# Performance work log

Hardware: AMD Instinct MI355X
Metric: run time of the kernel (lower is better)

## Reference

```python
import jax, jax.numpy as jnp
import numpy as np

N_NODES = 50000
N_EDGES = 800000
N_GRAPHS = 64
EMB_DIM = 24
N_KERNELS = 2
M_DIM = 64
FOURIER = 4
POS_DIM = 3
EDGE_IN = 2 * FOURIER + 1 + 2 * EMB_DIM  # 57
MLP_DIM = 256
N_OUT = 4
FFNN_IN = EMB_DIM * (N_KERNELS + 1)  # 72


def _lin(key, fan_in, fan_out, stack=None):
    # xavier-uniform weight, zero bias (matches weights_init)
    lim = (6.0 / (fan_in + fan_out)) ** 0.5
    shp = ((stack,) if stack else ()) + (fan_in, fan_out)
    w = jax.random.uniform(key, shp, minval=-lim, maxval=lim, dtype=jnp.float32)
    b = jnp.zeros(((stack,) if stack else ()) + (fan_out,), jnp.float32)
    return w, b


def setup_inputs() -> dict:
    key = jax.random.key(0)
    ks = jax.random.split(key, 20)
    z = jax.random.randint(ks[0], (N_NODES,), 0, 22)
    pos = jax.random.normal(ks[1], (N_NODES, POS_DIM), jnp.float32)
    edge_index = jax.random.randint(ks[2], (2, N_EDGES), 0, N_NODES)
    batch_idx = jnp.sort(jax.random.randint(ks[3], (N_NODES,), 0, N_GRAPHS))
    lim_e = (6.0 / (22 + EMB_DIM)) ** 0.5
    emb_table = jax.random.uniform(ks[4], (22, EMB_DIM), minval=-lim_e, maxval=lim_e, dtype=jnp.float32)
    emb_w, emb_b = _lin(ks[5], EMB_DIM, EMB_DIM)
    # EGNN kernel params, stacked over N_KERNELS
    ew1, eb1 = _lin(ks[6], EDGE_IN, EDGE_IN * 2, N_KERNELS)
    ew2, eb2 = _lin(ks[7], EDGE_IN * 2, M_DIM, N_KERNELS)
    cw1, cb1 = _lin(ks[8], M_DIM, M_DIM * 4, N_KERNELS)
    cw2, cb2 = _lin(ks[9], M_DIM * 4, 1, N_KERNELS)
    nw1, nb1 = _lin(ks[10], EMB_DIM + M_DIM, EMB_DIM * 2, N_KERNELS)
    nw2, nb2 = _lin(ks[11], EMB_DIM * 2, EMB_DIM, N_KERNELS)
    # ffnn: Linear(72,256), Linear(256,256), Linear(256,256), Linear(256,4)
    f0w, f0b = _lin(ks[12], FFNN_IN, MLP_DIM)
    f1w, f1b = _lin(ks[13], MLP_DIM, MLP_DIM)
    f2w, f2b = _lin(ks[14], MLP_DIM, MLP_DIM)
    fow, fob = _lin(ks[15], MLP_DIM, N_OUT)
    return dict(z=z, pos=pos, edge_index=edge_index, batch_idx=batch_idx,
                emb_table=emb_table, emb_w=emb_w, emb_b=emb_b,
                ew1=ew1, eb1=eb1, ew2=ew2, eb2=eb2,
                cw1=cw1, cb1=cb1, cw2=cw2, cb2=cb2,
                nw1=nw1, nb1=nb1, nw2=nw2, nb2=nb2,
                f0w=f0w, f0b=f0b, f1w=f1w, f1b=f1b, f2w=f2w, f2b=f2b,
                fow=fow, fob=fob)


def _egnn_layer(feats, coors, src, dst, ew1, eb1, ew2, eb2, cw1, cb1, cw2, cb2, nw1, nb1, nw2, nb2):
    # EGNN_sparse (PyG flow source_to_target: i=dst=edge_index[1], j=src=edge_index[0])
    rel = coors[src] - coors[dst]                       # [E,3]
    d = jnp.sum(rel * rel, axis=-1, keepdims=True)      # [E,1] squared distance
    scales = 2.0 ** jnp.arange(FOURIER, dtype=feats.dtype)
    ds = d / scales                                     # [E,4]
    edge_feat = jnp.concatenate([jnp.sin(ds), jnp.cos(ds), d], axis=-1)  # [E,9]
    e_in = jnp.concatenate([feats[dst], feats[src], edge_feat], axis=-1)  # [E,57]
    m_ij = jax.nn.silu(jax.nn.silu(e_in @ ew1 + eb1) @ ew2 + eb2)         # [E,64]
    coor_w = jax.nn.silu(m_ij @ cw1 + cb1) @ cw2 + cb2                    # [E,1]
    coors_out = coors + jax.ops.segment_sum(coor_w * rel, dst, num_segments=N_NODES)
    m_i = jax.ops.segment_sum(m_ij, dst, num_segments=N_NODES)            # [N,64]
    h = jax.nn.silu(jnp.concatenate([feats, m_i], axis=-1) @ nw1 + nb1)
    feats_out = feats + (h @ nw2 + nb2)
    return feats_out, coors_out


def reference(z, pos, edge_index, batch_idx, emb_table, emb_w, emb_b,
              ew1, eb1, ew2, eb2, cw1, cb1, cw2, cb2, nw1, nb1, nw2, nb2,
              f0w, f0b, f1w, f1b, f2w, f2b, fow, fob):
    src, dst = edge_index[0], edge_index[1]
    feats = emb_table[z] @ emb_w + emb_b
    coors = pos
    flist = [feats]
    for k in range(N_KERNELS):
        feats, coors = _egnn_layer(feats, coors, src, dst,
                                   ew1[k], eb1[k], ew2[k], eb2[k],
                                   cw1[k], cb1[k], cw2[k], cb2[k],
                                   nw1[k], nb1[k], nw2[k], nb2[k])
        flist.append(feats)
    x = jax.nn.silu(jnp.concatenate(flist, axis=-1))     # [N,72]
    x = jax.nn.silu(x @ f0w + f0b)
    x = jax.nn.silu(x @ f1w + f1b)
    x = jax.nn.silu(x @ f2w + f2b)                       # [N,256]
    cnt = jax.ops.segment_sum(jnp.ones((x.shape[0],), x.dtype), batch_idx, num_segments=N_GRAPHS)
    pooled = jax.ops.segment_sum(x, batch_idx, num_segments=N_GRAPHS) / jnp.maximum(cnt, 1.0)[:, None]
    return jax.nn.sigmoid(pooled @ fow + fob)            # [B,4]
```

## Files before the change

kernel.cpp:

```cpp
#include <hip/hip_runtime.h>
#include <hip/hip_bf16.h>

#define N_NODES  50000
#define N_EDGES  800000
#define N_GRAPHS 64
#define EMB      24
#define MDIM     64
#define EDGE_IN  57
#define EH       114
#define CH       256
#define NIN      88
#define NH       48
#define MLP      256
#define ETILE    128
#define NTILE    64

typedef __bf16 bf16_t;
typedef __bf16 bf16x8 __attribute__((ext_vector_type(8)));
typedef __bf16 bf16x4 __attribute__((ext_vector_type(4)));
typedef float  f32x4  __attribute__((ext_vector_type(4)));

__device__ __forceinline__ float siluf(float x) {
    return x * __builtin_amdgcn_rcpf(1.0f + __expf(-x));
}

__global__ void embed_kernel(const int* __restrict__ z, const float* __restrict__ table,
                             const float* __restrict__ w, const float* __restrict__ b,
                             const int* __restrict__ batch, float* __restrict__ f0,
                             bf16_t* __restrict__ fb0, float* __restrict__ cnt)
{
    int n = blockIdx.x * blockDim.x + threadIdx.x;
    if (n >= N_NODES) return;
    float r[EMB];
    const float4* tr = reinterpret_cast<const float4*>(table + z[n] * EMB);
    #pragma unroll
    for (int q = 0; q < 6; q++) {
        float4 v = tr[q];
        r[q*4] = v.x; r[q*4+1] = v.y; r[q*4+2] = v.z; r[q*4+3] = v.w;
    }
    float o[EMB];
    #pragma unroll
    for (int j = 0; j < EMB; j++) o[j] = b[j];
    #pragma unroll
    for (int i = 0; i < EMB; i++) {
        #pragma unroll
        for (int j = 0; j < EMB; j++) o[j] = fmaf(r[i], w[i*EMB + j], o[j]);
    }
    float4* dst = reinterpret_cast<float4*>(f0 + (size_t)n * EMB);
    #pragma unroll
    for (int q = 0; q < 6; q++) dst[q] = make_float4(o[q*4], o[q*4+1], o[q*4+2], o[q*4+3]);
    bf16x8* bdst = reinterpret_cast<bf16x8*>(fb0 + (size_t)n * EMB);
    #pragma unroll
    for (int q = 0; q < 3; q++) {
        bf16x8 pk;
        #pragma unroll
        for (int j = 0; j < 8; j++) pk[j] = (bf16_t)o[q*8 + j];
        bdst[q] = pk;
    }
    atomicAdd(&cnt[batch[n]], 1.0f);
}

#define PK_W1   (128*64)
#define PK_W2   (64*128)
#define PK_CW   (256*64)
#define PK_F0   (256*128)
#define PK_FM   (256*256)
#define PK_TOT  (2*PK_W1 + 2*PK_W2 + PK_CW + PK_F0 + 2*PK_FM)
__global__ void pack_kernel(const float* __restrict__ ew1, const float* __restrict__ eb1,
                            const float* __restrict__ ew2, const float* __restrict__ eb2,
                            const float* __restrict__ cw1, const float* __restrict__ f0w,
                            const float* __restrict__ f1w, const float* __restrict__ f2w,
                            bf16_t* __restrict__ pw)
{
    int idx = blockIdx.x * blockDim.x + threadIdx.x;
    if (idx >= PK_TOT) return;
    float v = 0.0f;
    if (idx < 2 * PK_W1) {
        int l = idx / PK_W1, r = idx - l * PK_W1;
        int n = r >> 6, k = r & 63;
        if (n < EH && k < EDGE_IN)       v = ew1[(l * EDGE_IN + k) * EH + n];
        else if (n < EH && k == EDGE_IN) v = eb1[l * EH + n];
    } else if (idx < 2 * PK_W1 + 2 * PK_W2) {
        int r0 = idx - 2 * PK_W1;
        int l = r0 / PK_W2, r = r0 - l * PK_W2;
        int n = r >> 7, k = r & 127;
        if (k < EH)       v = ew2[(l * EH + k) * MDIM + n];
        else if (k == EH) v = eb2[l * MDIM + n];
    } else if (idx < 2 * PK_W1 + 2 * PK_W2 + PK_CW) {
        int r = idx - (2 * PK_W1 + 2 * PK_W2);
        int n = r >> 6, k = r & 63;
        v = cw1[k * CH + n];
    } else if (idx < 2 * PK_W1 + 2 * PK_W2 + PK_CW + PK_F0) {
        int r = idx - (2 * PK_W1 + 2 * PK_W2 + PK_CW);
        int n = r >> 7, k = r & 127;
        if (k < 72) v = f0w[k * MLP + n];
    } else {
        int r0 = idx - (2 * PK_W1 + 2 * PK_W2 + PK_CW + PK_F0);
        int l = r0 / PK_FM, r = r0 - l * PK_FM;
        int n = r >> 8, k = r & 255;
        v = (l == 0) ? f1w[k * MLP + n] : f2w[k * MLP + n];
    }
    pw[idx] = (bf16_t)v;
}

__global__ void hist_kernel(const int* __restrict__ dst, int* __restrict__ deg)
{
    int e = blockIdx.x * blockDim.x + threadIdx.x;
    if (e < N_EDGES) atomicAdd(&deg[dst[e]], 1);
}

__global__ __launch_bounds__(1024)
void scan_kernel(const int* __restrict__ deg, int* __restrict__ cursor)
{
    __shared__ int part[1024];
    int t = threadIdx.x;
    const int PER = 49;
    int base = t * PER;
    int s = 0;
    for (int i = 0; i < PER; i++) {
        int p = base + i;
        if (p < N_NODES) s += deg[p];
    }
    part[t] = s;
    __syncthreads();
    for (int off = 1; off < 1024; off <<= 1) {
        int add = (t >= off) ? part[t - off] : 0;
        __syncthreads();
        part[t] += add;
        __syncthreads();
    }
    int run = (t > 0) ? part[t - 1] : 0;
    for (int i = 0; i < PER; i++) {
        int p = base + i;
        if (p < N_NODES) { cursor[p] = run; run += deg[p]; }
    }
}

__global__ void scatter_kernel(const int* __restrict__ src, const int* __restrict__ dst,
                               int* __restrict__ cursor, int* __restrict__ srcs_s,
                               int* __restrict__ dsts_s)
{
    int e = blockIdx.x * blockDim.x + threadIdx.x;
    if (e >= N_EDGES) return;
    int d = dst[e];
    int pos = atomicAdd(&cursor[d], 1);
    srcs_s[pos] = src[e];
    dsts_s[pos] = d;
}

template<int COOR>
__global__ __launch_bounds__(256, 4)
void edge_mfma(const bf16_t* __restrict__ fb, const float* __restrict__ coors,
               const int* __restrict__ srcs_s, const int* __restrict__ dsts_s,
               const bf16_t* __restrict__ W1t, const bf16_t* __restrict__ W2t,
               const bf16_t* __restrict__ CW1t, const float* __restrict__ cb1,
               const float* __restrict__ cw2, const float* __restrict__ cb2,
               float* __restrict__ m_i, float* __restrict__ cdelta)
{
    __shared__ __align__(16) char R1raw[ETILE * 64 * 4];
    __shared__ float s_rel[COOR ? ETILE * 3 : 4];
    __shared__ float s_cacc[COOR ? ETILE : 4];
    __shared__ int   s_dst[ETILE];
    bf16_t* R1 = (bf16_t*)R1raw;
    float*  Mf32 = (float*)R1raw;

    const int t = threadIdx.x;
    const int w = t >> 6;
    const int l = t & 63;
    const int row0 = w * 32;
    const int ebase = blockIdx.x * ETILE;
    const int l15 = l & 15, l4 = l >> 4;

    {
        int e_loc = t >> 1, half = t & 1;
        int e = ebase + e_loc;
        int s = srcs_s[e], d = dsts_s[e];
        if (half == 0) {
            s_dst[e_loc] = d;
            const bf16x8* fp = reinterpret_cast<const bf16x8*>(fb + (size_t)d * EMB);
            #pragma unroll
            for (int g = 0; g < 3; g++)
                *(bf16x8*)&R1[e_loc*64 + (g ^ (e_loc & 7))*8] = fp[g];
        } else {
            const bf16x8* fp = reinterpret_cast<const bf16x8*>(fb + (size_t)s * EMB);
            #pragma unroll
            for (int g = 0; g < 3; g++)
                *(bf16x8*)&R1[e_loc*64 + ((g + 3) ^ (e_loc & 7))*8] = fp[g];
            float rx = coors[s*3+0] - coors[d*3+0];
            float ry = coors[s*3+1] - coors[d*3+1];
            float rz = coors[s*3+2] - coors[d*3+2];
            float d2 = rx*rx + ry*ry + rz*rz;
            if (COOR) { s_rel[e_loc*3+0] = rx; s_rel[e_loc*3+1] = ry; s_rel[e_loc*3+2] = rz; }
            bf16x8 p6, p7;
            p6[0]=(bf16_t)__sinf(d2);        p6[1]=(bf16_t)__sinf(d2*0.5f);
            p6[2]=(bf16_t)__sinf(d2*0.25f);  p6[3]=(bf16_t)__sinf(d2*0.125f);
            p6[4]=(bf16_t)__cosf(d2);        p6[5]=(bf16_t)__cosf(d2*0.5f);
            p6[6]=(bf16_t)__cosf(d2*0.25f);  p6[7]=(bf16_t)__cosf(d2*0.125f);
            p7[0]=(bf16_t)d2; p7[1]=(bf16_t)1.0f;
            p7[2]=(bf16_t)0.f; p7[3]=(bf16_t)0.f; p7[4]=(bf16_t)0.f;
            p7[5]=(bf16_t)0.f; p7[6]=(bf16_t)0.f; p7[7]=(bf16_t)0.f;
            *(bf16x8*)&R1[e_loc*64 + (6 ^ (e_loc & 7))*8] = p6;
            *(bf16x8*)&R1[e_loc*64 + (7 ^ (e_loc & 7))*8] = p7;
        }
    }
    __syncthreads();

    f32x4 acc1[2][8];
    #pragma unroll
    for (int et = 0; et < 2; et++)
        #pragma unroll
        for (int ft = 0; ft < 8; ft++) acc1[et][ft] = (f32x4){0.f,0.f,0.f,0.f};
    #pragma unroll
    for (int ks = 0; ks < 2; ks++) {
        bf16x8 bfrag[2];
        #pragma unroll
        for (int et = 0; et < 2; et++) {
            int e = row0 + et*16 + l15;
            bfrag[et] = *(const bf16x8*)&R1[e*64 + ((ks*4 + l4) ^ (e & 7))*8];
        }
        #pragma unroll
        for (int ft = 0; ft < 8; ft++) {
            bf16x8 a = *(const bf16x8*)&W1t[(ft*16 + l15)*64 + (ks*4 + l4)*8];
            acc1[0][ft] = __builtin_amdgcn_mfma_f32_16x16x32_bf16(a, bfrag[0], acc1[0][ft], 0, 0, 0);
            acc1[1][ft] = __builtin_amdgcn_mfma_f32_16x16x32_bf16(a, bfrag[1], acc1[1][ft], 0, 0, 0);
        }
    }
    __syncthreads();
    #pragma unroll
    for (int et = 0; et < 2; et++)
        #pragma unroll
        for (int ft = 0; ft < 8; ft++) {
            int e = row0 + et*16 + l15;
            int f0 = ft*16 + l4*4;
            bf16x4 pk;
            #pragma unroll
            for (int r4 = 0; r4 < 4; r4++) {
                float hv = siluf(acc1[et][ft][r4]);
                if (f0 + r4 == EH) hv = 1.0f;
                pk[r4] = (bf16_t)hv;
            }
            *(bf16x4*)&R1[e*128 + ((f0 >> 3) ^ (e & 7))*8 + (f0 & 7)] = pk;
        }
    __syncthreads();

    f32x4 acc2[2][4];
    #pragma unroll
    for (int et = 0; et < 2; et++)
        #pragma unroll
        for (int ft = 0; ft < 4; ft++) acc2[et][ft] = (f32x4){0.f,0.f,0.f,0.f};
    #pragma unroll
    for (int ks = 0; ks < 4; ks++) {
        bf16x8 bfrag[2];
        #pragma unroll
        for (int et = 0; et < 2; et++) {
            int e = row0 + et*16 + l15;
            bfrag[et] = *(const bf16x8*)&R1[e*128 + ((ks*4 + l4) ^ (e & 7))*8];
        }
        #pragma unroll
        for (int ft = 0; ft < 4; ft++) {
            bf16x8 a = *(const bf16x8*)&W2t[(ft*16 + l15)*128 + (ks*4 + l4)*8];
            acc2[0][ft] = __builtin_amdgcn_mfma_f32_16x16x32_bf16(a, bfrag[0], acc2[0][ft], 0, 0, 0);
            acc2[1][ft] = __builtin_amdgcn_mfma_f32_16x16x32_bf16(a, bfrag[1], acc2[1][ft], 0, 0, 0);
        }
    }
    __syncthreads();
    #pragma unroll
    for (int et = 0; et < 2; et++)
        #pragma unroll
        for (int ft = 0; ft < 4; ft++) {
            int e = row0 + et*16 + l15;
            int f0 = ft*16 + l4*4;
            f32x4 v;
            #pragma unroll
            for (int r4 = 0; r4 < 4; r4++) v[r4] = siluf(acc2[et][ft][r4]);
            *(f32x4*)&Mf32[e*64 + (((f0 >> 2) ^ (e & 7)) << 2)] = v;
        }
    __syncthreads();

    {
        int col = t & 63;
        int gsw_base = col >> 2, cw = col & 3;
        int gb = w * 32;
        int cur = s_dst[gb];
        float run = 0.f;
        for (int i = 0; i < 32; i++) {
            int row = gb + i;
            int d = s_dst[row];
            float v = Mf32[row*64 + ((gsw_base ^ (row & 7)) << 2) + cw];
            if (d != cur) { atomicAdd(&m_i[(size_t)cur*64 + col], run); run = 0.f; cur = d; }
            run += v;
        }
        atomicAdd(&m_i[(size_t)cur*64 + col], run);
    }

    if (COOR) {
        float csum[2] = {0.f, 0.f};
        #pragma unroll
        for (int half = 0; half < 2; half++) {
            f32x4 acc3[2][8];
            #pragma unroll
            for (int et = 0; et < 2; et++)
                #pragma unroll
                for (int ft = 0; ft < 8; ft++) acc3[et][ft] = (f32x4){0.f,0.f,0.f,0.f};
            #pragma unroll
            for (int ks = 0; ks < 2; ks++) {
                bf16x8 bfrag[2];
                #pragma unroll
                for (int et = 0; et < 2; et++) {
                    int e = row0 + et*16 + l15;
                    int g0 = (ks*4 + l4) * 2;
                    f32x4 lo = *(const f32x4*)&Mf32[e*64 + ((g0 ^ (e & 7)) << 2)];
                    f32x4 hi = *(const f32x4*)&Mf32[e*64 + (((g0 + 1) ^ (e & 7)) << 2)];
                    bf16x8 bk;
                    #pragma unroll
                    for (int j = 0; j < 4; j++) { bk[j] = (bf16_t)lo[j]; bk[j+4] = (bf16_t)hi[j]; }
                    bfrag[et] = bk;
                }
                #pragma unroll
                for (int ft = 0; ft < 8; ft++) {
                    bf16x8 a = *(const bf16x8*)&CW1t[(half*128 + ft*16 + l15)*64 + (ks*4 + l4)*8];
                    acc3[0][ft] = __builtin_amdgcn_mfma_f32_16x16x32_bf16(a, bfrag[0], acc3[0][ft], 0, 0, 0);
                    acc3[1][ft] = __builtin_amdgcn_mfma_f32_16x16x32_bf16(a, bfrag[1], acc3[1][ft], 0, 0, 0);
                }
            }
            #pragma unroll
            for (int ft = 0; ft < 8; ft++) {
                int f0 = half*128 + ft*16 + l4*4;
                float4 c1 = *(const float4*)&cb1[f0];
                float4 w2 = *(const float4*)&cw2[f0];
                #pragma unroll
                for (int et = 0; et < 2; et++) {
                    csum[et] = fmaf(siluf(acc3[et][ft][0] + c1.x), w2.x, csum[et]);
                    csum[et] = fmaf(siluf(acc3[et][ft][1] + c1.y), w2.y, csum[et]);
                    csum[et] = fmaf(siluf(acc3[et][ft][2] + c1.z), w2.z, csum[et]);
                    csum[et] = fmaf(siluf(acc3[et][ft][3] + c1.w), w2.w, csum[et]);
                }
            }
        }
        #pragma unroll
        for (int et = 0; et < 2; et++) {
            csum[et] += __shfl_xor(csum[et], 16);
            csum[et] += __shfl_xor(csum[et], 32);
        }
        if (l < 16) {
            float cb2v = cb2[0];
            s_cacc[row0 + l]      = csum[0] + cb2v;
            s_cacc[row0 + 16 + l] = csum[1] + cb2v;
        }
        __syncthreads();
        if (t < ETILE) {
            int d = s_dst[t];
            bool head = (t == 0) || (s_dst[t-1] != d);
            if (head) {
                float ax = 0.f, ay = 0.f, az = 0.f;
                int i = t;
                do {
                    float c = s_cacc[i];
                    ax = fmaf(c, s_rel[i*3+0], ax);
                    ay = fmaf(c, s_rel[i*3+1], ay);
                    az = fmaf(c, s_rel[i*3+2], az);
                    ++i;
                } while (i < ETILE && s_dst[i] == d);
                atomicAdd(&cdelta[d*3+0], ax);
                atomicAdd(&cdelta[d*3+1], ay);
                atomicAdd(&cdelta[d*3+2], az);
            }
        }
    }
}

template<int EMIT_BF16>
__global__ __launch_bounds__(256)
void node_kernel(const float* __restrict__ feats, const float* __restrict__ m_i,
                 const float* __restrict__ nw1, const float* __restrict__ nb1,
                 const float* __restrict__ nw2, const float* __restrict__ nb2,
                 float* __restrict__ fout, bf16_t* __restrict__ fbout)
{
    __shared__ float s_w1t[NH * NIN];
    __shared__ float s_b1[NH];
    __shared__ float s_w2[NH * EMB];
    __shared__ float s_b2[EMB];
    const int tid = threadIdx.x;
    for (int idx = tid; idx < NH * NIN; idx += 256) {
        int k = idx / NIN, i = idx - k * NIN;
        s_w1t[idx] = nw1[i * NH + k];
    }
    for (int idx = tid; idx < NH * EMB; idx += 256) s_w2[idx] = nw2[idx];
    if (tid < NH) s_b1[tid] = nb1[tid];
    if (tid < EMB) s_b2[tid] = nb2[tid];
    __syncthreads();

    int n = blockIdx.x * 256 + tid;
    if (n >= N_NODES) return;

    float in[NIN];
    const float4* fp = reinterpret_cast<const float4*>(feats + (size_t)n * EMB);
    #pragma unroll
    for (int q = 0; q < 6; q++) {
        float4 v = fp[q];
        in[q*4] = v.x; in[q*4+1] = v.y; in[q*4+2] = v.z; in[q*4+3] = v.w;
    }
    const float4* mp = reinterpret_cast<const float4*>(m_i + (size_t)n * MDIM);
    #pragma unroll
    for (int q = 0; q < 16; q++) {
        float4 v = mp[q];
        in[EMB+q*4] = v.x; in[EMB+q*4+1] = v.y; in[EMB+q*4+2] = v.z; in[EMB+q*4+3] = v.w;
    }
    float o[EMB];
    #pragma unroll
    for (int j = 0; j < EMB; j++) o[j] = in[j] + s_b2[j];
    for (int k = 0; k < NH; k++) {
        const float* w1 = &s_w1t[k * NIN];
        float a0 = 0.f, a1 = 0.f, a2 = 0.f, a3 = 0.f;
        #pragma unroll
        for (int i = 0; i < NIN; i += 4) {
            a0 = fmaf(in[i],   w1[i],   a0);
            a1 = fmaf(in[i+1], w1[i+1], a1);
            a2 = fmaf(in[i+2], w1[i+2], a2);
            a3 = fmaf(in[i+3], w1[i+3], a3);
        }
        float h = siluf(s_b1[k] + ((a0 + a1) + (a2 + a3)));
        const float* w2 = &s_w2[k * EMB];
        #pragma unroll
        for (int j = 0; j < EMB; j++) o[j] = fmaf(h, w2[j], o[j]);
    }
    float4* dst = reinterpret_cast<float4*>(fout + (size_t)n * EMB);
    #pragma unroll
    for (int q = 0; q < 6; q++) dst[q] = make_float4(o[q*4], o[q*4+1], o[q*4+2], o[q*4+3]);
    if (EMIT_BF16) {
        bf16x8* bdst = reinterpret_cast<bf16x8*>(fbout + (size_t)n * EMB);
        #pragma unroll
        for (int q = 0; q < 3; q++) {
            bf16x8 pk;
            #pragma unroll
            for (int j = 0; j < 8; j++) pk[j] = (bf16_t)o[q*8 + j];
            bdst[q] = pk;
        }
    }
}

__global__ void coor_kernel(const float* __restrict__ pos, const float* __restrict__ cdelta,
                            float* __restrict__ out)
{
    int i = blockIdx.x * blockDim.x + threadIdx.x;
    if (i < N_NODES * 3) out[i] = pos[i] + cdelta[i];
}

__global__ __launch_bounds__(512, 4)
void ffnn_fused(const float* __restrict__ f0, const float* __restrict__ f1,
                const float* __restrict__ f2,
                const bf16_t* __restrict__ W0p, const bf16_t* __restrict__ W1p,
                const bf16_t* __restrict__ W2p,
                const float* __restrict__ b0, const float* __restrict__ b1,
                const float* __restrict__ b2,
                const int* __restrict__ batch, float* __restrict__ pooled)
{
    __shared__ __align__(16) bf16_t sH[NTILE * 256];
    __shared__ int s_batch[NTILE];
    const int t = threadIdx.x;
    const int w = t >> 6, l = t & 63;
    const int l15 = l & 15, q = l >> 4;
    const int mt = w & 3;
    const int nh = w >> 2;
    const int mrow0 = mt * 16;
    const int n0 = blockIdx.x * NTILE;

    {
        int row = t >> 3, part = t & 7;
        int n = n0 + row;
        bool valid = n < N_NODES;
        if (part == 7) s_batch[row] = valid ? batch[n] : -1;
        #pragma unroll
        for (int gi = 0; gi < 2; gi++) {
            int g = part * 2 + gi;
            bf16x8 pk;
            #pragma unroll
            for (int j = 0; j < 8; j++) pk[j] = (bf16_t)0.f;
            if (valid && g < 9) {
                const float* sp = (g < 3) ? f0 + (size_t)n*EMB + 8*g
                                : (g < 6) ? f1 + (size_t)n*EMB + 8*(g-3)
                                          : f2 + (size_t)n*EMB + 8*(g-6);
                float4 a = ((const float4*)sp)[0], b = ((const float4*)sp)[1];
                pk[0]=(bf16_t)siluf(a.x); pk[1]=(bf16_t)siluf(a.y);
                pk[2]=(bf16_t)siluf(a.z); pk[3]=(bf16_t)siluf(a.w);
                pk[4]=(bf16_t)siluf(b.x); pk[5]=(bf16_t)siluf(b.y);
                pk[6]=(bf16_t)siluf(b.z); pk[7]=(bf16_t)siluf(b.w);
            }
            *(bf16x8*)&sH[row*128 + (g ^ (row & 7))*8] = pk;
        }
    }
    __syncthreads();

    bf16x8 a0[4];
    {
        int r = mrow0 + l15;
        #pragma unroll
        for (int ks = 0; ks < 4; ks++)
            a0[ks] = *(const bf16x8*)&sH[r*128 + ((ks*4 + q) ^ (r & 7))*8];
    }
    __syncthreads();

    f32x4 acc[8];
    #pragma unroll
    for (int nt = 0; nt < 8; nt++) {
        float bv = b0[(nh*8 + nt)*16 + l15];
        acc[nt] = (f32x4){bv, bv, bv, bv};
    }
    #pragma unroll
    for (int ks = 0; ks < 4; ks++)
        #pragma unroll
        for (int nt = 0; nt < 8; nt++) {
            int n = (nh*8 + nt)*16 + l15;
            bf16x8 b = *(const bf16x8*)&W0p[n*128 + (ks*4 + q)*8];
            acc[nt] = __builtin_amdgcn_mfma_f32_16x16x32_bf16(a0[ks], b, acc[nt], 0, 0, 0);
        }
    #pragma unroll
    for (int nt = 0; nt < 8; nt++)
        #pragma unroll
        for (int r4 = 0; r4 < 4; r4++) {
            int row = mrow0 + q*4 + r4;
            int col = (nh*8 + nt)*16 + l15;
            sH[row*256 + ((col >> 3) ^ (row & 7))*8 + (col & 7)] = (bf16_t)siluf(acc[nt][r4]);
        }
    __syncthreads();

    #pragma unroll
    for (int layer = 0; layer < 2; layer++) {
        const bf16_t* Wp = layer ? W2p : W1p;
        const float*  bb = layer ? b2  : b1;
        #pragma unroll
        for (int nt = 0; nt < 8; nt++) {
            float bv = bb[(nh*8 + nt)*16 + l15];
            acc[nt] = (f32x4){bv, bv, bv, bv};
        }
        for (int ks = 0; ks < 8; ks++) {
            int r = mrow0 + l15;
            bf16x8 a = *(const bf16x8*)&sH[r*256 + ((ks*4 + q) ^ (r & 7))*8];
            #pragma unroll
            for (int nt = 0; nt < 8; nt++) {
                int n = (nh*8 + nt)*16 + l15;
                bf16x8 b = *(const bf16x8*)&Wp[n*256 + (ks*4 + q)*8];
                acc[nt] = __builtin_amdgcn_mfma_f32_16x16x32_bf16(a, b, acc[nt], 0, 0, 0);
            }
        }
        __syncthreads();
        #pragma unroll
        for (int nt = 0; nt < 8; nt++)
            #pragma unroll
            for (int r4 = 0; r4 < 4; r4++) {
                int row = mrow0 + q*4 + r4;
                int col = (nh*8 + nt)*16 + l15;
                sH[row*256 + ((col >> 3) ^ (row & 7))*8 + (col & 7)] = (bf16_t)siluf(acc[nt][r4]);
            }
        __syncthreads();
    }

    {
        int j = t & 255;
        int rh = t >> 8;
        int g = j >> 3, jo = j & 7;
        int cur = -1;
        float run = 0.f;
        for (int i = rh*32; i < rh*32 + 32; i++) {
            int bb = s_batch[i];
            if (bb != cur) {
                if (cur >= 0) atomicAdd(&pooled[cur * MLP + j], run);
                run = 0.f; cur = bb;
            }
            if (bb >= 0) run += (float)sH[i*256 + (g ^ (i & 7))*8 + jo];
        }
        if (cur >= 0) atomicAdd(&pooled[cur * MLP + j], run);
    }
}

__global__ void final_kernel(const float* __restrict__ pooled, const float* __restrict__ cnt,
                             const float* __restrict__ fow, const float* __restrict__ fob,
                             float* __restrict__ out)
{
    int t = threadIdx.x;
    int bg = t >> 2, o = t & 3;
    float c = fmaxf(cnt[bg], 1.0f);
    float acc = 0.f;
    for (int i = 0; i < MLP; i++) acc = fmaf(pooled[bg * MLP + i], fow[i * 4 + o], acc);
    acc = acc / c + fob[o];
    out[t] = 1.0f / (1.0f + __expf(-acc));
}

extern "C" void kernel_launch(void* const* d_in, const int* in_sizes, int n_in,
                              void* d_out, int out_size, void* d_ws, size_t ws_size,
                              hipStream_t stream)
{
    const int*   z     = (const int*)  d_in[0];
    const float* pos   = (const float*)d_in[1];
    const int*   eidx  = (const int*)  d_in[2];
    const int*   batch = (const int*)  d_in[3];
    const float* embt  = (const float*)d_in[4];
    const float* embw  = (const float*)d_in[5];
    const float* embb  = (const float*)d_in[6];
    const float* ew1   = (const float*)d_in[7];
    const float* eb1   = (const float*)d_in[8];
    const float* ew2   = (const float*)d_in[9];
    const float* eb2   = (const float*)d_in[10];
    const float* cw1   = (const float*)d_in[11];
    const float* cb1   = (const float*)d_in[12];
    const float* cw2   = (const float*)d_in[13];
    const float* cb2   = (const float*)d_in[14];
    const float* nw1   = (const float*)d_in[15];
    const float* nb1   = (const float*)d_in[16];
    const float* nw2   = (const float*)d_in[17];
    const float* nb2   = (const float*)d_in[18];
    const float* f0w   = (const float*)d_in[19];
    const float* f0b   = (const float*)d_in[20];
    const float* f1w   = (const float*)d_in[21];
    const float* f1b   = (const float*)d_in[22];
    const float* f2w   = (const float*)d_in[23];
    const float* f2b   = (const float*)d_in[24];
    const float* fow   = (const float*)d_in[25];
    const float* fob   = (const float*)d_in[26];

    float* ws     = (float*)d_ws;
    float* f0     = ws;
    float* f1v    = f0 + (size_t)N_NODES * EMB;
    float* f2v    = f1v + (size_t)N_NODES * EMB;
    bf16_t* fb0   = (bf16_t*)(f2v + (size_t)N_NODES * EMB);
    bf16_t* fb1   = fb0 + (size_t)N_NODES * EMB;
    float* coorsA = (float*)(fb1 + (size_t)N_NODES * EMB);
    float* cdelta = coorsA + N_NODES * 3;
    float* m_i    = cdelta + N_NODES * 3;
    float* pooled = m_i + (size_t)N_NODES * MDIM;
    float* cnt    = pooled + N_GRAPHS * MLP;
    int*   deg    = (int*)(cnt + N_GRAPHS);
    int*   cursor = deg + N_NODES;
    int*   srcs_s = cursor + N_NODES;
    int*   dsts_s = srcs_s + N_EDGES;
    bf16_t* packw = (bf16_t*)(dsts_s + N_EDGES);
    bf16_t* W1t0  = packw;
    bf16_t* W1t1  = W1t0 + PK_W1;
    bf16_t* W2t0  = W1t1 + PK_W1;
    bf16_t* W2t1  = W2t0 + PK_W2;
    bf16_t* CW1t  = W2t1 + PK_W2;
    bf16_t* W0p   = CW1t + PK_CW;
    bf16_t* W1p   = W0p + PK_F0;
    bf16_t* W2p   = W1p + PK_FM;

    hipMemsetAsync(cdelta, 0, N_NODES * 3 * sizeof(float), stream);
    hipMemsetAsync(m_i, 0, (size_t)N_NODES * MDIM * sizeof(float), stream);
    hipMemsetAsync(pooled, 0, (N_GRAPHS * MLP + N_GRAPHS) * sizeof(float), stream);
    hipMemsetAsync(deg, 0, N_NODES * sizeof(int), stream);

    const int* e_src = eidx;
    const int* e_dst = eidx + N_EDGES;
    pack_kernel<<<(PK_TOT + 255) / 256, 256, 0, stream>>>(ew1, eb1, ew2, eb2, cw1,
                                                          f0w, f1w, f2w, packw);
    hist_kernel<<<(N_EDGES + 255) / 256, 256, 0, stream>>>(e_dst, deg);
    scan_kernel<<<1, 1024, 0, stream>>>(deg, cursor);
    scatter_kernel<<<(N_EDGES + 255) / 256, 256, 0, stream>>>(e_src, e_dst, cursor, srcs_s, dsts_s);

    embed_kernel<<<(N_NODES + 255) / 256, 256, 0, stream>>>(z, embt, embw, embb, batch, f0, fb0, cnt);

    const int EBLK = N_EDGES / ETILE;
    edge_mfma<1><<<EBLK, 256, 0, stream>>>(fb0, pos, srcs_s, dsts_s,
        W1t0, W2t0, CW1t, cb1, cw2, cb2, m_i, cdelta);
    node_kernel<1><<<(N_NODES + 255) / 256, 256, 0, stream>>>(f0, m_i, nw1, nb1, nw2, nb2, f1v, fb1);
    coor_kernel<<<(N_NODES * 3 + 255) / 256, 256, 0, stream>>>(pos, cdelta, coorsA);
    hipMemsetAsync(m_i, 0, (size_t)N_NODES * MDIM * sizeof(float), stream);
    edge_mfma<0><<<EBLK, 256, 0, stream>>>(fb1, coorsA, srcs_s, dsts_s,
        W1t1, W2t1, CW1t, cb1, cw2, cb2, m_i, nullptr);
    node_kernel<0><<<(N_NODES + 255) / 256, 256, 0, stream>>>(f1v, m_i,
        nw1 + NIN * NH, nb1 + NH, nw2 + NH * EMB, nb2 + EMB, f2v, nullptr);

    const int FBLK = (N_NODES + NTILE - 1) / NTILE;
    ffnn_fused<<<FBLK, 512, 0, stream>>>(f0, f1v, f2v, W0p, W1p, W2p,
                                         f0b, f1b, f2b, batch, pooled);

    final_kernel<<<1, 256, 0, stream>>>(pooled, cnt, fow, fob, (float*)d_out);
}
```

Baseline: 995.4 us.

## Use 512-thread edge blocks with one 16-edge MFMA tile per wave

Doubles the edge kernel's block size to 8 waves, so each wave now processes 16 edges instead of 32, which halves per-wave accumulator registers. The gather phase is split four ways per edge: dst features, src features, sin/cos features, and d2 plus relative coordinates. The aim is higher occupancy and more parallel memory latency hiding. In exchange, each W1/W2/CW1 weight fragment load is reused across half as many MFMAs, and the coordinate distance is computed redundantly by two threads.

```diff
diff --git a/kernel.cpp b/kernel.cpp
--- a/kernel.cpp
+++ b/kernel.cpp
@@ -149,7 +149,7 @@
 }
 
 template<int COOR>
-__global__ __launch_bounds__(256, 4)
+__global__ __launch_bounds__(512, 8)
 void edge_mfma(const bf16_t* __restrict__ fb, const float* __restrict__ coors,
                const int* __restrict__ srcs_s, const int* __restrict__ dsts_s,
                const bf16_t* __restrict__ W1t, const bf16_t* __restrict__ W2t,
@@ -167,123 +167,112 @@
     const int t = threadIdx.x;
     const int w = t >> 6;
     const int l = t & 63;
-    const int row0 = w * 32;
+    const int row0 = w * 16;
     const int ebase = blockIdx.x * ETILE;
     const int l15 = l & 15, l4 = l >> 4;
 
     {
-        int e_loc = t >> 1, half = t & 1;
+        int e_loc = t >> 2, part = t & 3;
         int e = ebase + e_loc;
-        int s = srcs_s[e], d = dsts_s[e];
-        if (half == 0) {
+        if (part == 0) {
+            int d = dsts_s[e];
             s_dst[e_loc] = d;
             const bf16x8* fp = reinterpret_cast<const bf16x8*>(fb + (size_t)d * EMB);
             #pragma unroll
             for (int g = 0; g < 3; g++)
                 *(bf16x8*)&R1[e_loc*64 + (g ^ (e_loc & 7))*8] = fp[g];
-        } else {
+        } else if (part == 1) {
+            int s = srcs_s[e];
             const bf16x8* fp = reinterpret_cast<const bf16x8*>(fb + (size_t)s * EMB);
             #pragma unroll
             for (int g = 0; g < 3; g++)
                 *(bf16x8*)&R1[e_loc*64 + ((g + 3) ^ (e_loc & 7))*8] = fp[g];
+        } else {
+            int s = srcs_s[e], d = dsts_s[e];
             float rx = coors[s*3+0] - coors[d*3+0];
             float ry = coors[s*3+1] - coors[d*3+1];
             float rz = coors[s*3+2] - coors[d*3+2];
             float d2 = rx*rx + ry*ry + rz*rz;
-            if (COOR) { s_rel[e_loc*3+0] = rx; s_rel[e_loc*3+1] = ry; s_rel[e_loc*3+2] = rz; }
-            bf16x8 p6, p7;
-            p6[0]=(bf16_t)__sinf(d2);        p6[1]=(bf16_t)__sinf(d2*0.5f);
-            p6[2]=(bf16_t)__sinf(d2*0.25f);  p6[3]=(bf16_t)__sinf(d2*0.125f);
-            p6[4]=(bf16_t)__cosf(d2);        p6[5]=(bf16_t)__cosf(d2*0.5f);
-            p6[6]=(bf16_t)__cosf(d2*0.25f);  p6[7]=(bf16_t)__cosf(d2*0.125f);
-            p7[0]=(bf16_t)d2; p7[1]=(bf16_t)1.0f;
-            p7[2]=(bf16_t)0.f; p7[3]=(bf16_t)0.f; p7[4]=(bf16_t)0.f;
-            p7[5]=(bf16_t)0.f; p7[6]=(bf16_t)0.f; p7[7]=(bf16_t)0.f;
-            *(bf16x8*)&R1[e_loc*64 + (6 ^ (e_loc & 7))*8] = p6;
-            *(bf16x8*)&R1[e_loc*64 + (7 ^ (e_loc & 7))*8] = p7;
-        }
-    }
-    __syncthreads();
-
-    f32x4 acc1[2][8];
-    #pragma unroll
-    for (int et = 0; et < 2; et++)
-        #pragma unroll
-        for (int ft = 0; ft < 8; ft++) acc1[et][ft] = (f32x4){0.f,0.f,0.f,0.f};
+            if (part == 2) {
+                bf16x8 p6;
+                p6[0]=(bf16_t)__sinf(d2);        p6[1]=(bf16_t)__sinf(d2*0.5f);
+                p6[2]=(bf16_t)__sinf(d2*0.25f);  p6[3]=(bf16_t)__sinf(d2*0.125f);
+                p6[4]=(bf16_t)__cosf(d2);        p6[5]=(bf16_t)__cosf(d2*0.5f);
+                p6[6]=(bf16_t)__cosf(d2*0.25f);  p6[7]=(bf16_t)__cosf(d2*0.125f);
+                *(bf16x8*)&R1[e_loc*64 + (6 ^ (e_loc & 7))*8] = p6;
+            } else {
+                if (COOR) { s_rel[e_loc*3+0] = rx; s_rel[e_loc*3+1] = ry; s_rel[e_loc*3+2] = rz; }
+                bf16x8 p7;
+                p7[0]=(bf16_t)d2; p7[1]=(bf16_t)1.0f;
+                p7[2]=(bf16_t)0.f; p7[3]=(bf16_t)0.f; p7[4]=(bf16_t)0.f;
+                p7[5]=(bf16_t)0.f; p7[6]=(bf16_t)0.f; p7[7]=(bf16_t)0.f;
+                *(bf16x8*)&R1[e_loc*64 + (7 ^ (e_loc & 7))*8] = p7;
+            }
+        }
+    }
+    __syncthreads();
+
+    f32x4 acc1[8];
+    #pragma unroll
+    for (int ft = 0; ft < 8; ft++) acc1[ft] = (f32x4){0.f,0.f,0.f,0.f};
     #pragma unroll
     for (int ks = 0; ks < 2; ks++) {
-        bf16x8 bfrag[2];
-        #pragma unroll
-        for (int et = 0; et < 2; et++) {
-            int e = row0 + et*16 + l15;
-            bfrag[et] = *(const bf16x8*)&R1[e*64 + ((ks*4 + l4) ^ (e & 7))*8];
-        }
+        int e = row0 + l15;
+        bf16x8 bfrag = *(const bf16x8*)&R1[e*64 + ((ks*4 + l4) ^ (e & 7))*8];
         #pragma unroll
         for (int ft = 0; ft < 8; ft++) {
             bf16x8 a = *(const bf16x8*)&W1t[(ft*16 + l15)*64 + (ks*4 + l4)*8];
-            acc1[0][ft] = __builtin_amdgcn_mfma_f32_16x16x32_bf16(a, bfrag[0], acc1[0][ft], 0, 0, 0);
-            acc1[1][ft] = __builtin_amdgcn_mfma_f32_16x16x32_bf16(a, bfrag[1], acc1[1][ft], 0, 0, 0);
-        }
-    }
-    __syncthreads();
-    #pragma unroll
-    for (int et = 0; et < 2; et++)
-        #pragma unroll
-        for (int ft = 0; ft < 8; ft++) {
-            int e = row0 + et*16 + l15;
-            int f0 = ft*16 + l4*4;
-            bf16x4 pk;
-            #pragma unroll
-            for (int r4 = 0; r4 < 4; r4++) {
-                float hv = siluf(acc1[et][ft][r4]);
-                if (f0 + r4 == EH) hv = 1.0f;
-                pk[r4] = (bf16_t)hv;
-            }
-            *(bf16x4*)&R1[e*128 + ((f0 >> 3) ^ (e & 7))*8 + (f0 & 7)] = pk;
-        }
-    __syncthreads();
-
-    f32x4 acc2[2][4];
-    #pragma unroll
-    for (int et = 0; et < 2; et++)
-        #pragma unroll
-        for (int ft = 0; ft < 4; ft++) acc2[et][ft] = (f32x4){0.f,0.f,0.f,0.f};
+            acc1[ft] = __builtin_amdgcn_mfma_f32_16x16x32_bf16(a, bfrag, acc1[ft], 0, 0, 0);
+        }
+    }
+    __syncthreads();
+    #pragma unroll
+    for (int ft = 0; ft < 8; ft++) {
+        int e = row0 + l15;
+        int f0 = ft*16 + l4*4;
+        bf16x4 pk;
+        #pragma unroll
+        for (int r4 = 0; r4 < 4; r4++) {
+            float hv = siluf(acc1[ft][r4]);
+            if (f0 + r4 == EH) hv = 1.0f;
+            pk[r4] = (bf16_t)hv;
+        }
+        *(bf16x4*)&R1[e*128 + ((f0 >> 3) ^ (e & 7))*8 + (f0 & 7)] = pk;
+    }
+    __syncthreads();
+
+    f32x4 acc2[4];
+    #pragma unroll
+    for (int ft = 0; ft < 4; ft++) acc2[ft] = (f32x4){0.f,0.f,0.f,0.f};
     #pragma unroll
     for (int ks = 0; ks < 4; ks++) {
-        bf16x8 bfrag[2];
-        #pragma unroll
-        for (int et = 0; et < 2; et++) {
-            int e = row0 + et*16 + l15;
-            bfrag[et] = *(const bf16x8*)&R1[e*128 + ((ks*4 + l4) ^ (e & 7))*8];
-        }
+        int e = row0 + l15;
+        bf16x8 bfrag = *(const bf16x8*)&R1[e*128 + ((ks*4 + l4) ^ (e & 7))*8];
         #pragma unroll
         for (int ft = 0; ft < 4; ft++) {
             bf16x8 a = *(const bf16x8*)&W2t[(ft*16 + l15)*128 + (ks*4 + l4)*8];
-            acc2[0][ft] = __builtin_amdgcn_mfma_f32_16x16x32_bf16(a, bfrag[0], acc2[0][ft], 0, 0, 0);
-            acc2[1][ft] = __builtin_amdgcn_mfma_f32_16x16x32_bf16(a, bfrag[1], acc2[1][ft], 0, 0, 0);
-        }
-    }
-    __syncthreads();
-    #pragma unroll
-    for (int et = 0; et < 2; et++)
-        #pragma unroll
-        for (int ft = 0; ft < 4; ft++) {
-            int e = row0 + et*16 + l15;
-            int f0 = ft*16 + l4*4;
-            f32x4 v;
-            #pragma unroll
-            for (int r4 = 0; r4 < 4; r4++) v[r4] = siluf(acc2[et][ft][r4]);
-            *(f32x4*)&Mf32[e*64 + (((f0 >> 2) ^ (e & 7)) << 2)] = v;
-        }
+            acc2[ft] = __builtin_amdgcn_mfma_f32_16x16x32_bf16(a, bfrag, acc2[ft], 0, 0, 0);
+        }
+    }
+    __syncthreads();
+    #pragma unroll
+    for (int ft = 0; ft < 4; ft++) {
+        int e = row0 + l15;
+        int f0 = ft*16 + l4*4;
+        f32x4 v;
+        #pragma unroll
+        for (int r4 = 0; r4 < 4; r4++) v[r4] = siluf(acc2[ft][r4]);
+        *(f32x4*)&Mf32[e*64 + (((f0 >> 2) ^ (e & 7)) << 2)] = v;
+    }
     __syncthreads();
 
     {
         int col = t & 63;
         int gsw_base = col >> 2, cw = col & 3;
-        int gb = w * 32;
+        int gb = (t >> 6) * 16;
         int cur = s_dst[gb];
         float run = 0.f;
-        for (int i = 0; i < 32; i++) {
+        for (int i = 0; i < 16; i++) {
             int row = gb + i;
             int d = s_dst[row];
             float v = Mf32[row*64 + ((gsw_base ^ (row & 7)) << 2) + cw];
@@ -294,33 +283,25 @@
     }
 
     if (COOR) {
-        float csum[2] = {0.f, 0.f};
+        float csum = 0.f;
         #pragma unroll
         for (int half = 0; half < 2; half++) {
-            f32x4 acc3[2][8];
-            #pragma unroll
-            for (int et = 0; et < 2; et++)
+            f32x4 acc3[8];
+            #pragma unroll
+            for (int ft = 0; ft < 8; ft++) acc3[ft] = (f32x4){0.f,0.f,0.f,0.f};
+            #pragma unroll
+            for (int ks = 0; ks < 2; ks++) {
+                int e = row0 + l15;
+                int g0 = (ks*4 + l4) * 2;
+                f32x4 lo = *(const f32x4*)&Mf32[e*64 + ((g0 ^ (e & 7)) << 2)];
+                f32x4 hi = *(const f32x4*)&Mf32[e*64 + (((g0 + 1) ^ (e & 7)) << 2)];
+                bf16x8 bfrag;
                 #pragma unroll
-                for (int ft = 0; ft < 8; ft++) acc3[et][ft] = (f32x4){0.f,0.f,0.f,0.f};
-            #pragma unroll
-            for (int ks = 0; ks < 2; ks++) {
-                bf16x8 bfrag[2];
-                #pragma unroll
-                for (int et = 0; et < 2; et++) {
-                    int e = row0 + et*16 + l15;
-                    int g0 = (ks*4 + l4) * 2;
-                    f32x4 lo = *(const f32x4*)&Mf32[e*64 + ((g0 ^ (e & 7)) << 2)];
-                    f32x4 hi = *(const f32x4*)&Mf32[e*64 + (((g0 + 1) ^ (e & 7)) << 2)];
-                    bf16x8 bk;
-                    #pragma unroll
-                    for (int j = 0; j < 4; j++) { bk[j] = (bf16_t)lo[j]; bk[j+4] = (bf16_t)hi[j]; }
-                    bfrag[et] = bk;
-                }
+                for (int j = 0; j < 4; j++) { bfrag[j] = (bf16_t)lo[j]; bfrag[j+4] = (bf16_t)hi[j]; }
                 #pragma unroll
                 for (int ft = 0; ft < 8; ft++) {
                     bf16x8 a = *(const bf16x8*)&CW1t[(half*128 + ft*16 + l15)*64 + (ks*4 + l4)*8];
-                    acc3[0][ft] = __builtin_amdgcn_mfma_f32_16x16x32_bf16(a, bfrag[0], acc3[0][ft], 0, 0, 0);
-                    acc3[1][ft] = __builtin_amdgcn_mfma_f32_16x16x32_bf16(a, bfrag[1], acc3[1][ft], 0, 0, 0);
+                    acc3[ft] = __builtin_amdgcn_mfma_f32_16x16x32_bf16(a, bfrag, acc3[ft], 0, 0, 0);
                 }
             }
             #pragma unroll
@@ -328,24 +309,16 @@
                 int f0 = half*128 + ft*16 + l4*4;
                 float4 c1 = *(const float4*)&cb1[f0];
                 float4 w2 = *(const float4*)&cw2[f0];
-                #pragma unroll
-                for (int et = 0; et < 2; et++) {
-                    csum[et] = fmaf(siluf(acc3[et][ft][0] + c1.x), w2.x, csum[et]);
-                    csum[et] = fmaf(siluf(acc3[et][ft][1] + c1.y), w2.y, csum[et]);
-                    csum[et] = fmaf(siluf(acc3[et][ft][2] + c1.z), w2.z, csum[et]);
-                    csum[et] = fmaf(siluf(acc3[et][ft][3] + c1.w), w2.w, csum[et]);
-                }
-            }
-        }
-        #pragma unroll
-        for (int et = 0; et < 2; et++) {
-            csum[et] += __shfl_xor(csum[et], 16);
-            csum[et] += __shfl_xor(csum[et], 32);
-        }
+                csum = fmaf(siluf(acc3[ft][0] + c1.x), w2.x, csum);
+                csum = fmaf(siluf(acc3[ft][1] + c1.y), w2.y, csum);
+                csum = fmaf(siluf(acc3[ft][2] + c1.z), w2.z, csum);
+                csum = fmaf(siluf(acc3[ft][3] + c1.w), w2.w, csum);
+            }
+        }
+        csum += __shfl_xor(csum, 16);
+        csum += __shfl_xor(csum, 32);
         if (l < 16) {
-            float cb2v = cb2[0];
-            s_cacc[row0 + l]      = csum[0] + cb2v;
-            s_cacc[row0 + 16 + l] = csum[1] + cb2v;
+            s_cacc[row0 + l] = csum + cb2[0];
         }
         __syncthreads();
         if (t < ETILE) {
@@ -659,12 +632,12 @@
     embed_kernel<<<(N_NODES + 255) / 256, 256, 0, stream>>>(z, embt, embw, embb, batch, f0, fb0, cnt);
 
     const int EBLK = N_EDGES / ETILE;
-    edge_mfma<1><<<EBLK, 256, 0, stream>>>(fb0, pos, srcs_s, dsts_s,
+    edge_mfma<1><<<EBLK, 512, 0, stream>>>(fb0, pos, srcs_s, dsts_s,
         W1t0, W2t0, CW1t, cb1, cw2, cb2, m_i, cdelta);
     node_kernel<1><<<(N_NODES + 255) / 256, 256, 0, stream>>>(f0, m_i, nw1, nb1, nw2, nb2, f1v, fb1);
     coor_kernel<<<(N_NODES * 3 + 255) / 256, 256, 0, stream>>>(pos, cdelta, coorsA);
     hipMemsetAsync(m_i, 0, (size_t)N_NODES * MDIM * sizeof(float), stream);
-    edge_mfma<0><<<EBLK, 256, 0, stream>>>(fb1, coorsA, srcs_s, dsts_s,
+    edge_mfma<0><<<EBLK, 512, 0, stream>>>(fb1, coorsA, srcs_s, dsts_s,
         W1t1, W2t1, CW1t, cb1, cw2, cb2, m_i, nullptr);
     node_kernel<0><<<(N_NODES + 255) / 256, 256, 0, stream>>>(f1v, m_i,
         nw1 + NIN * NH, nb1 + NH, nw2 + NH * EMB, nb2 + EMB, f2v, nullptr);
```

Measured after the change: 1.257 ms. +26.3%, slower.

## Give each wave a private LDS slab and drop block-wide barriers in edge kernel

Applied to the files above, without the earlier changes.

Each of the four waves in the edge kernel already gathers and processes its own 32 edges, so the shared staging buffer is split into one 8 KB slab per wave. All block-level __syncthreads in the edge MLP and coordinate path are removed. The coordinate segment reduction now runs per wave over 32 rows instead of per block over 128. This removes cross-wave stalls so waves can progress independently. In exchange it relies on in-wave ordering of LDS accesses and may issue a few more atomics where destination runs cross wave boundaries.

```diff
diff --git a/kernel.cpp b/kernel.cpp
--- a/kernel.cpp
+++ b/kernel.cpp
@@ -157,12 +157,10 @@
                const float* __restrict__ cw2, const float* __restrict__ cb2,
                float* __restrict__ m_i, float* __restrict__ cdelta)
 {
-    __shared__ __align__(16) char R1raw[ETILE * 64 * 4];
+    __shared__ __align__(16) char R1raw[4 * 8192];
     __shared__ float s_rel[COOR ? ETILE * 3 : 4];
     __shared__ float s_cacc[COOR ? ETILE : 4];
     __shared__ int   s_dst[ETILE];
-    bf16_t* R1 = (bf16_t*)R1raw;
-    float*  Mf32 = (float*)R1raw;
 
     const int t = threadIdx.x;
     const int w = t >> 6;
@@ -170,9 +168,12 @@
     const int row0 = w * 32;
     const int ebase = blockIdx.x * ETILE;
     const int l15 = l & 15, l4 = l >> 4;
+    bf16_t* slab16 = (bf16_t*)(R1raw + w * 8192);
+    float*  slab32 = (float*) (R1raw + w * 8192);
 
     {
         int e_loc = t >> 1, half = t & 1;
+        int e_l = e_loc & 31;
         int e = ebase + e_loc;
         int s = srcs_s[e], d = dsts_s[e];
         if (half == 0) {
@@ -180,12 +181,12 @@
             const bf16x8* fp = reinterpret_cast<const bf16x8*>(fb + (size_t)d * EMB);
             #pragma unroll
             for (int g = 0; g < 3; g++)
-                *(bf16x8*)&R1[e_loc*64 + (g ^ (e_loc & 7))*8] = fp[g];
+                *(bf16x8*)&slab16[e_l*64 + (g ^ (e_l & 7))*8] = fp[g];
         } else {
             const bf16x8* fp = reinterpret_cast<const bf16x8*>(fb + (size_t)s * EMB);
             #pragma unroll
             for (int g = 0; g < 3; g++)
-                *(bf16x8*)&R1[e_loc*64 + ((g + 3) ^ (e_loc & 7))*8] = fp[g];
+                *(bf16x8*)&slab16[e_l*64 + ((g + 3) ^ (e_l & 7))*8] = fp[g];
             float rx = coors[s*3+0] - coors[d*3+0];
             float ry = coors[s*3+1] - coors[d*3+1];
             float rz = coors[s*3+2] - coors[d*3+2];
@@ -199,11 +200,10 @@
             p7[0]=(bf16_t)d2; p7[1]=(bf16_t)1.0f;
             p7[2]=(bf16_t)0.f; p7[3]=(bf16_t)0.f; p7[4]=(bf16_t)0.f;
             p7[5]=(bf16_t)0.f; p7[6]=(bf16_t)0.f; p7[7]=(bf16_t)0.f;
-            *(bf16x8*)&R1[e_loc*64 + (6 ^ (e_loc & 7))*8] = p6;
-            *(bf16x8*)&R1[e_loc*64 + (7 ^ (e_loc & 7))*8] = p7;
-        }
-    }
-    __syncthreads();
+            *(bf16x8*)&slab16[e_l*64 + (6 ^ (e_l & 7))*8] = p6;
+            *(bf16x8*)&slab16[e_l*64 + (7 ^ (e_l & 7))*8] = p7;
+        }
+    }
 
     f32x4 acc1[2][8];
     #pragma unroll
@@ -215,8 +215,8 @@
         bf16x8 bfrag[2];
         #pragma unroll
         for (int et = 0; et < 2; et++) {
-            int e = row0 + et*16 + l15;
-            bfrag[et] = *(const bf16x8*)&R1[e*64 + ((ks*4 + l4) ^ (e & 7))*8];
+            int e_l = et*16 + l15;
+            bfrag[et] = *(const bf16x8*)&slab16[e_l*64 + ((ks*4 + l4) ^ (e_l & 7))*8];
         }
         #pragma unroll
         for (int ft = 0; ft < 8; ft++) {
@@ -225,12 +225,11 @@
             acc1[1][ft] = __builtin_amdgcn_mfma_f32_16x16x32_bf16(a, bfrag[1], acc1[1][ft], 0, 0, 0);
         }
     }
-    __syncthreads();
     #pragma unroll
     for (int et = 0; et < 2; et++)
         #pragma unroll
         for (int ft = 0; ft < 8; ft++) {
-            int e = row0 + et*16 + l15;
+            int e_l = et*16 + l15;
             int f0 = ft*16 + l4*4;
             bf16x4 pk;
             #pragma unroll
@@ -239,9 +238,8 @@
                 if (f0 + r4 == EH) hv = 1.0f;
                 pk[r4] = (bf16_t)hv;
             }
-            *(bf16x4*)&R1[e*128 + ((f0 >> 3) ^ (e & 7))*8 + (f0 & 7)] = pk;
-        }
-    __syncthreads();
+            *(bf16x4*)&slab16[e_l*128 + ((f0 >> 3) ^ (e_l & 7))*8 + (f0 & 7)] = pk;
+        }
 
     f32x4 acc2[2][4];
     #pragma unroll
@@ -253,8 +251,8 @@
         bf16x8 bfrag[2];
         #pragma unroll
         for (int et = 0; et < 2; et++) {
-            int e = row0 + et*16 + l15;
-            bfrag[et] = *(const bf16x8*)&R1[e*128 + ((ks*4 + l4) ^ (e & 7))*8];
+            int e_l = et*16 + l15;
+            bfrag[et] = *(const bf16x8*)&slab16[e_l*128 + ((ks*4 + l4) ^ (e_l & 7))*8];
         }
         #pragma unroll
         for (int ft = 0; ft < 4; ft++) {
@@ -263,30 +261,26 @@
             acc2[1][ft] = __builtin_amdgcn_mfma_f32_16x16x32_bf16(a, bfrag[1], acc2[1][ft], 0, 0, 0);
         }
     }
-    __syncthreads();
     #pragma unroll
     for (int et = 0; et < 2; et++)
         #pragma unroll
         for (int ft = 0; ft < 4; ft++) {
-            int e = row0 + et*16 + l15;
+            int e_l = et*16 + l15;
             int f0 = ft*16 + l4*4;
             f32x4 v;
             #pragma unroll
             for (int r4 = 0; r4 < 4; r4++) v[r4] = siluf(acc2[et][ft][r4]);
-            *(f32x4*)&Mf32[e*64 + (((f0 >> 2) ^ (e & 7)) << 2)] = v;
-        }
-    __syncthreads();
+            *(f32x4*)&slab32[e_l*64 + (((f0 >> 2) ^ (e_l & 7)) << 2)] = v;
+        }
 
     {
-        int col = t & 63;
+        int col = l;
         int gsw_base = col >> 2, cw = col & 3;
-        int gb = w * 32;
-        int cur = s_dst[gb];
+        int cur = s_dst[row0];
         float run = 0.f;
         for (int i = 0; i < 32; i++) {
-            int row = gb + i;
-            int d = s_dst[row];
-            float v = Mf32[row*64 + ((gsw_base ^ (row & 7)) << 2) + cw];
+            int d = s_dst[row0 + i];
+            float v = slab32[i*64 + ((gsw_base ^ (i & 7)) << 2) + cw];
             if (d != cur) { atomicAdd(&m_i[(size_t)cur*64 + col], run); run = 0.f; cur = d; }
             run += v;
         }
@@ -294,7 +288,7 @@
     }
 
     if (COOR) {
-        float csum[2] = {0.f, 0.f};
+        float csum0 = 0.f, csum1 = 0.f;
         #pragma unroll
         for (int half = 0; half < 2; half++) {
             f32x4 acc3[2][8];
@@ -307,10 +301,10 @@
                 bf16x8 bfrag[2];
                 #pragma unroll
                 for (int et = 0; et < 2; et++) {
-                    int e = row0 + et*16 + l15;
+                    int e_l = et*16 + l15;
                     int g0 = (ks*4 + l4) * 2;
-                    f32x4 lo = *(const f32x4*)&Mf32[e*64 + ((g0 ^ (e & 7)) << 2)];
-                    f32x4 hi = *(const f32x4*)&Mf32[e*64 + (((g0 + 1) ^ (e & 7)) << 2)];
+                    f32x4 lo = *(const f32x4*)&slab32[e_l*64 + ((g0 ^ (e_l & 7)) << 2)];
+                    f32x4 hi = *(const f32x4*)&slab32[e_l*64 + (((g0 + 1) ^ (e_l & 7)) << 2)];
                     bf16x8 bk;
                     #pragma unroll
                     for (int j = 0; j < 4; j++) { bk[j] = (bf16_t)lo[j]; bk[j+4] = (bf16_t)hi[j]; }
@@ -328,39 +322,39 @@
                 int f0 = half*128 + ft*16 + l4*4;
                 float4 c1 = *(const float4*)&cb1[f0];
                 float4 w2 = *(const float4*)&cw2[f0];
-                #pragma unroll
-                for (int et = 0; et < 2; et++) {
-                    csum[et] = fmaf(siluf(acc3[et][ft][0] + c1.x), w2.x, csum[et]);
-                    csum[et] = fmaf(siluf(acc3[et][ft][1] + c1.y), w2.y, csum[et]);
-                    csum[et] = fmaf(siluf(acc3[et][ft][2] + c1.z), w2.z, csum[et]);
-                    csum[et] = fmaf(siluf(acc3[et][ft][3] + c1.w), w2.w, csum[et]);
-                }
-            }
-        }
-        #pragma unroll
-        for (int et = 0; et < 2; et++) {
-            csum[et] += __shfl_xor(csum[et], 16);
-            csum[et] += __shfl_xor(csum[et], 32);
-        }
-        if (l < 16) {
-            float cb2v = cb2[0];
-            s_cacc[row0 + l]      = csum[0] + cb2v;
-            s_cacc[row0 + 16 + l] = csum[1] + cb2v;
-        }
-        __syncthreads();
-        if (t < ETILE) {
-            int d = s_dst[t];
-            bool head = (t == 0) || (s_dst[t-1] != d);
+                csum0 = fmaf(siluf(acc3[0][ft][0] + c1.x), w2.x, csum0);
+                csum0 = fmaf(siluf(acc3[0][ft][1] + c1.y), w2.y, csum0);
+                csum0 = fmaf(siluf(acc3[0][ft][2] + c1.z), w2.z, csum0);
+                csum0 = fmaf(siluf(acc3[0][ft][3] + c1.w), w2.w, csum0);
+                csum1 = fmaf(siluf(acc3[1][ft][0] + c1.x), w2.x, csum1);
+                csum1 = fmaf(siluf(acc3[1][ft][1] + c1.y), w2.y, csum1);
+                csum1 = fmaf(siluf(acc3[1][ft][2] + c1.z), w2.z, csum1);
+                csum1 = fmaf(siluf(acc3[1][ft][3] + c1.w), w2.w, csum1);
+            }
+        }
+        csum0 += __shfl_xor(csum0, 16);
+        csum0 += __shfl_xor(csum0, 32);
+        csum1 += __shfl_xor(csum1, 16);
+        csum1 += __shfl_xor(csum1, 32);
+        float cb2v = cb2[0];
+        if (l < 32) {
+            s_cacc[row0 + l] = ((l & 16) ? csum1 : csum0) + cb2v;
+        }
+        if (l < 32) {
+            int row = row0 + l;
+            int d = s_dst[row];
+            bool head = (l == 0) || (s_dst[row - 1] != d);
             if (head) {
                 float ax = 0.f, ay = 0.f, az = 0.f;
-                int i = t;
+                int i = l;
                 do {
-                    float c = s_cacc[i];
-                    ax = fmaf(c, s_rel[i*3+0], ax);
-                    ay = fmaf(c, s_rel[i*3+1], ay);
-                    az = fmaf(c, s_rel[i*3+2], az);
+                    int r = row0 + i;
+                    float c = s_cacc[r];
+                    ax = fmaf(c, s_rel[r*3+0], ax);
+                    ay = fmaf(c, s_rel[r*3+1], ay);
+                    az = fmaf(c, s_rel[r*3+2], az);
                     ++i;
-                } while (i < ETILE && s_dst[i] == d);
+                } while (i < 32 && s_dst[row0 + i] == d);
                 atomicAdd(&cdelta[d*3+0], ax);
                 atomicAdd(&cdelta[d*3+1], ay);
                 atomicAdd(&cdelta[d*3+2], az);
```

After: 972.4 us. 1.02x faster.
